# Performance work log

Measured on AMD Instinct MI355X. Metric: run time of the kernel, lower is better.

The kernel has to match this reference:

```python
import jax, jax.numpy as jnp
import numpy as np

BIG = 1e10
RADIUS = 0.5
NSAMPLE = 1


def square_distance(src, dst):
    # src: [B,N,3], dst: [B,M,3] -> [B,N,M] squared euclidean distances
    d = -2.0 * jnp.einsum('bnc,bmc->bnm', src, dst)
    d = d + jnp.sum(src ** 2, -1)[:, :, None]
    d = d + jnp.sum(dst ** 2, -1)[:, None, :]
    return d


def farthest_point_sample(xyz, npoint):
    # xyz: [B,N,3]; returns int32 indices [B,npoint]
    B, N, _ = xyz.shape
    dist0 = jnp.full((B, N), BIG, dtype=xyz.dtype)
    far0 = jnp.argmax(xyz[:, :, 0], axis=1).astype(jnp.int32)

    def step(carry, _):
        dist, far = carry
        centroid = jnp.take_along_axis(xyz, far[:, None, None], axis=1)  # [B,1,3]
        d = jnp.sum((xyz - centroid) ** 2, -1)  # [B,N]
        dist = jnp.minimum(dist, d)
        new_far = jnp.argmax(dist, axis=-1).astype(jnp.int32)
        return (dist, new_far), far  # record PRE-update farthest, like the torch loop

    (_, _), centroids = jax.lax.scan(step, (dist0, far0), None, length=npoint)
    return centroids.T  # [B,npoint]


def index_points(points, idx):
    # points: [B,N,C], idx: [B,S] -> [B,S,C]
    return jnp.take_along_axis(points, idx[:, :, None], axis=1)


def query_ball_point(radius, nsample, xyz, new_xyz):
    # xyz: [B,N,3], new_xyz: [B,S,3] -> int32 [B,S,nsample]
    B, S, _ = new_xyz.shape
    N = xyz.shape[1]
    sqrdists = square_distance(new_xyz, xyz)  # [B,S,N]
    base = jnp.arange(N, dtype=jnp.int32)
    group_idx = jnp.where(sqrdists > radius ** 2, jnp.int32(N), base)  # [B,S,N]
    group_idx = jnp.sort(group_idx, axis=-1)[:, :, :nsample]
    group_first = jnp.broadcast_to(group_idx[:, :, :1], group_idx.shape)
    group_idx = jnp.where(group_idx == N, group_first, group_idx)
    return group_idx


def setup_inputs() -> dict:
    key = jax.random.key(0)
    k1, k2 = jax.random.split(key)
    B, N = 4, 16384
    xyz = jax.random.uniform(k1, (B, 3, N), dtype=jnp.float32)
    cls_label = jax.random.uniform(k2, (B, 16), dtype=jnp.float32)
    return {"xyz": xyz, "cls_label": cls_label, "npoint": 1024}


def reference(xyz, cls_label, npoint):
    pts = jnp.transpose(xyz, (0, 2, 1))  # [B,N,3]
    centroids = farthest_point_sample(pts, npoint)  # [B,S]
    new_xyz = index_points(pts, centroids)  # [B,S,3]
    idx = query_ball_point(RADIUS, NSAMPLE, pts, new_xyz)  # [B,S,1]
    return idx
```

## Files before the change

kernel.cpp:

```cpp
#include <hip/hip_runtime.h>


constexpr int N_PTS  = 16384;
constexpr int NPOINT = 1024;
constexpr int BLOCK  = 512;
constexpr int KPT    = N_PTS / BLOCK;
constexpr int KP2    = KPT / 2;
constexpr int NWAVE  = BLOCK / 64;

typedef float f32x2 __attribute__((ext_vector_type(2)));

__device__ inline f32x2 pk_add(f32x2 a, f32x2 b) {
    f32x2 d;
    asm("v_pk_add_f32 %0, %1, %2" : "=v"(d) : "v"(a), "v"(b));
    return d;
}
__device__ inline f32x2 pk_mul(f32x2 a, f32x2 b) {
    f32x2 d;
    asm("v_pk_mul_f32 %0, %1, %2" : "=v"(d) : "v"(a), "v"(b));
    return d;
}

__device__ inline unsigned long long pack_key(float v, int idx) {
    return ((unsigned long long)__float_as_uint(v) << 32) |
           (unsigned)(N_PTS - 1 - idx);
}
__device__ inline int key_idx(unsigned long long k) {
    return N_PTS - 1 - (int)(k & 0xFFFFu);
}
__device__ inline unsigned long long umax64(unsigned long long a,
                                            unsigned long long b) {
    return a > b ? a : b;
}

__global__ __launch_bounds__(BLOCK, 2) void fps_kernel(
    const float* __restrict__ xyz,
    int* __restrict__ cent)
{
    const int b   = blockIdx.x;
    const int tid = threadIdx.x;
    const float* X = xyz + (size_t)b * 3 * N_PTS;
    const float* Y = X + N_PTS;
    const float* Z = X + 2 * N_PTS;

    f32x2 px[KP2], py[KP2], pz[KP2], dd[KP2];
#pragma unroll
    for (int k = 0; k < KP2; ++k) {
        const int p0 = tid + (2 * k) * BLOCK;
        const int p1 = tid + (2 * k + 1) * BLOCK;
        px[k] = f32x2{X[p0], X[p1]};
        py[k] = f32x2{Y[p0], Y[p1]};
        pz[k] = f32x2{Z[p0], Z[p1]};
        dd[k] = f32x2{1e10f, 1e10f};
    }
#pragma unroll
    for (int k = 0; k < KP2; ++k)
        asm("" : "+v"(px[k]), "+v"(py[k]), "+v"(pz[k]));

    __shared__ unsigned long long s_key[2][NWAVE];

    const int wave = tid >> 6;
    const int lane = tid & 63;

    int far;
    {
        float bv = px[0].x;
        int   bk = 0;
#pragma unroll
        for (int k = 0; k < KP2; ++k) {
            if (px[k].x > bv) { bv = px[k].x; bk = 2 * k; }
            if (px[k].y > bv) { bv = px[k].y; bk = 2 * k + 1; }
        }
        unsigned long long key = pack_key(bv, tid + bk * BLOCK);
#pragma unroll
        for (int off = 32; off > 0; off >>= 1)
            key = umax64(key, __shfl_xor(key, off));
        if (lane == 0) s_key[0][wave] = key;
        __syncthreads();
        const unsigned long long* sk = s_key[0];
        const unsigned long long bkk =
            umax64(umax64(umax64(sk[0], sk[1]), umax64(sk[2], sk[3])),
                   umax64(umax64(sk[4], sk[5]), umax64(sk[6], sk[7])));
        far = __builtin_amdgcn_readfirstlane(key_idx(bkk));
    }

    for (int it = 0; it < NPOINT; ++it) {
        if (tid == 0) cent[b * NPOINT + it] = far;
        if (it == NPOINT - 1) break;

        const float cx = X[far];
        const float cy = Y[far];
        const float cz = Z[far];
        const f32x2 ncx = {-cx, -cx};
        const f32x2 ncy = {-cy, -cy};
        const f32x2 ncz = {-cz, -cz};

        float nbv = -1.0f;
        int   nbk = 0;
#pragma unroll
        for (int k = 0; k < KP2; ++k) {
            const f32x2 dx = pk_add(px[k], ncx);
            const f32x2 dy = pk_add(py[k], ncy);
            const f32x2 dz = pk_add(pz[k], ncz);
            const f32x2 d  = pk_add(pk_add(pk_mul(dx, dx), pk_mul(dy, dy)),
                                    pk_mul(dz, dz));
            const float n0 = fminf(dd[k].x, d.x);
            const float n1 = fminf(dd[k].y, d.y);
            dd[k].x = n0;
            dd[k].y = n1;
            if (n0 > nbv) { nbv = n0; nbk = 2 * k; }
            if (n1 > nbv) { nbv = n1; nbk = 2 * k + 1; }
        }

        unsigned long long key = pack_key(nbv, tid + nbk * BLOCK);
#pragma unroll
        for (int off = 32; off > 0; off >>= 1)
            key = umax64(key, __shfl_xor(key, off));
        const int buf = (it + 1) & 1;
        if (lane == 0) s_key[buf][wave] = key;
        __syncthreads();

        const unsigned long long* sk = s_key[buf];
        const unsigned long long bkk =
            umax64(umax64(umax64(sk[0], sk[1]), umax64(sk[2], sk[3])),
                   umax64(umax64(sk[4], sk[5]), umax64(sk[6], sk[7])));
        far = __builtin_amdgcn_readfirstlane(key_idx(bkk));
    }
}

__global__ __launch_bounds__(256) void ballq_kernel(
    const float* __restrict__ xyz,
    const int* __restrict__ cent,
    int* __restrict__ out)
{
    const int gw   = (blockIdx.x * 256 + threadIdx.x) >> 6;
    const int lane = threadIdx.x & 63;
    const int b = gw / NPOINT;
    const int s = gw % NPOINT;

    const float* X = xyz + (size_t)b * 3 * N_PTS;
    const float* Y = X + N_PTS;
    const float* Z = X + 2 * N_PTS;

    const int ci = cent[b * NPOINT + s];
    const float cx = X[ci];
    const float cy = Y[ci];
    const float cz = Z[ci];
    const float cn = __fadd_rn(
        __fadd_rn(__fmul_rn(cx, cx), __fmul_rn(cy, cy)), __fmul_rn(cz, cz));

    int res = N_PTS;
    for (int base = 0; base < N_PTS; base += 64) {
        const int p = base + lane;
        const float x = X[p];
        const float y = Y[p];
        const float z = Z[p];
        const float dot = __fadd_rn(
            __fadd_rn(__fmul_rn(x, cx), __fmul_rn(y, cy)), __fmul_rn(z, cz));
        const float pn = __fadd_rn(
            __fadd_rn(__fmul_rn(x, x), __fmul_rn(y, y)), __fmul_rn(z, z));
        const float d = __fadd_rn(__fadd_rn(__fmul_rn(-2.0f, dot), cn), pn);
        const bool hit = !(d > 0.25f);
        const unsigned long long m = __ballot(hit);
        if (m) {
            res = base + (__ffsll((long long)m) - 1);
            break;
        }
    }
    if (lane == 0) out[b * NPOINT + s] = res;
}

extern "C" void kernel_launch(void* const* d_in, const int* in_sizes, int n_in,
                              void* d_out, int out_size, void* d_ws, size_t ws_size,
                              hipStream_t stream) {
    const float* xyz = (const float*)d_in[0];
    const int B = in_sizes[1] / 16;
    int* cent = (int*)d_ws;
    int* out  = (int*)d_out;

    fps_kernel<<<B, BLOCK, 0, stream>>>(xyz, cent);

    const int nwaves  = B * NPOINT;
    const int nblocks = nwaves / 4;
    ballq_kernel<<<nblocks, 256, 0, stream>>>(xyz, cent, out);
}
```

Baseline: 1.899 ms.

## Replace shuffle wave reduction with DPP max scan and split argmax chains

Replaces the six __shfl_xor 64-bit max-reduction steps in farthest point sampling with DPP row_shr/row_bcast steps, which avoid LDS-permute latency. The full wave result lands in lane 63. The per-thread argmax now uses two independent chains (even and odd slots) that are merged at the end, shortening the serial dependency in the inner loop. It also switches to the waves_per_eu attribute and masks indices defensively. DPP bank masks and lane ordering are subtle and could break tie-breaking if wrong.

```diff
diff --git a/kernel.cpp b/kernel.cpp
--- a/kernel.cpp
+++ b/kernel.cpp
@@ -33,7 +33,29 @@
     return a > b ? a : b;
 }
 
-__global__ __launch_bounds__(BLOCK, 2) void fps_kernel(
+template <int CTRL, int RM, int BM>
+__device__ inline unsigned long long dpp_max_step(unsigned long long key) {
+    const int lo = (int)(unsigned)key;
+    const int hi = (int)(unsigned)(key >> 32);
+    const unsigned mlo =
+        (unsigned)__builtin_amdgcn_update_dpp(lo, lo, CTRL, RM, BM, false);
+    const unsigned mhi =
+        (unsigned)__builtin_amdgcn_update_dpp(hi, hi, CTRL, RM, BM, false);
+    const unsigned long long moved = ((unsigned long long)mhi << 32) | mlo;
+    return key > moved ? key : moved;
+}
+__device__ inline unsigned long long wave_max_key(unsigned long long key) {
+    key = dpp_max_step<0x111, 0xf, 0xf>(key);
+    key = dpp_max_step<0x112, 0xf, 0xf>(key);
+    key = dpp_max_step<0x114, 0xf, 0xe>(key);
+    key = dpp_max_step<0x118, 0xf, 0xc>(key);
+    key = dpp_max_step<0x142, 0xa, 0xf>(key);
+    key = dpp_max_step<0x143, 0xc, 0xf>(key);
+    return key;
+}
+
+__global__ __launch_bounds__(BLOCK)
+__attribute__((amdgpu_waves_per_eu(2, 2))) void fps_kernel(
     const float* __restrict__ xyz,
     int* __restrict__ cent)
 {
@@ -55,7 +77,7 @@
     }
 #pragma unroll
     for (int k = 0; k < KP2; ++k)
-        asm("" : "+v"(px[k]), "+v"(py[k]), "+v"(pz[k]));
+        asm volatile("" : "+v"(px[k]), "+v"(py[k]), "+v"(pz[k]));
 
     __shared__ unsigned long long s_key[2][NWAVE];
 
@@ -71,17 +93,16 @@
             if (px[k].x > bv) { bv = px[k].x; bk = 2 * k; }
             if (px[k].y > bv) { bv = px[k].y; bk = 2 * k + 1; }
         }
-        unsigned long long key = pack_key(bv, tid + bk * BLOCK);
-#pragma unroll
-        for (int off = 32; off > 0; off >>= 1)
-            key = umax64(key, __shfl_xor(key, off));
-        if (lane == 0) s_key[0][wave] = key;
+        const unsigned long long key =
+            wave_max_key(pack_key(bv, tid + bk * BLOCK));
+        if (lane == 63) s_key[0][wave] = key;
         __syncthreads();
         const unsigned long long* sk = s_key[0];
         const unsigned long long bkk =
             umax64(umax64(umax64(sk[0], sk[1]), umax64(sk[2], sk[3])),
                    umax64(umax64(sk[4], sk[5]), umax64(sk[6], sk[7])));
-        far = __builtin_amdgcn_readfirstlane(key_idx(bkk));
+        far = __builtin_amdgcn_readfirstlane(key_idx(bkk)) &
+              (N_PTS - 1);
     }
 
     for (int it = 0; it < NPOINT; ++it) {
@@ -95,8 +116,8 @@
         const f32x2 ncy = {-cy, -cy};
         const f32x2 ncz = {-cz, -cz};
 
-        float nbv = -1.0f;
-        int   nbk = 0;
+        float bv0 = -1.0f, bv1 = -1.0f;
+        int   k0  = 0,     k1  = 1;
 #pragma unroll
         for (int k = 0; k < KP2; ++k) {
             const f32x2 dx = pk_add(px[k], ncx);
@@ -108,23 +129,26 @@
             const float n1 = fminf(dd[k].y, d.y);
             dd[k].x = n0;
             dd[k].y = n1;
-            if (n0 > nbv) { nbv = n0; nbk = 2 * k; }
-            if (n1 > nbv) { nbv = n1; nbk = 2 * k + 1; }
+            if (n0 > bv0) { bv0 = n0; k0 = 2 * k; }
+            if (n1 > bv1) { bv1 = n1; k1 = 2 * k + 1; }
         }
-
-        unsigned long long key = pack_key(nbv, tid + nbk * BLOCK);
-#pragma unroll
-        for (int off = 32; off > 0; off >>= 1)
-            key = umax64(key, __shfl_xor(key, off));
+        float nbv;
+        int   nbk;
+        if (bv1 > bv0 || (bv1 == bv0 && k1 < k0)) { nbv = bv1; nbk = k1; }
+        else                                      { nbv = bv0; nbk = k0; }
+
+        const unsigned long long key =
+            wave_max_key(pack_key(nbv, tid + (nbk << 9)));
         const int buf = (it + 1) & 1;
-        if (lane == 0) s_key[buf][wave] = key;
+        if (lane == 63) s_key[buf][wave] = key;
         __syncthreads();
 
         const unsigned long long* sk = s_key[buf];
         const unsigned long long bkk =
             umax64(umax64(umax64(sk[0], sk[1]), umax64(sk[2], sk[3])),
                    umax64(umax64(sk[4], sk[5]), umax64(sk[6], sk[7])));
-        far = __builtin_amdgcn_readfirstlane(key_idx(bkk));
+        far = __builtin_amdgcn_readfirstlane(key_idx(bkk)) &
+              (N_PTS - 1);
     }
 }
 
@@ -142,7 +166,7 @@
     const float* Y = X + N_PTS;
     const float* Z = X + 2 * N_PTS;
 
-    const int ci = cent[b * NPOINT + s];
+    const int ci = cent[b * NPOINT + s] & (N_PTS - 1);
     const float cx = X[ci];
     const float cy = Y[ci];
     const float cz = Z[ci];
```

Measured after the change: 1.785 ms. -6.0%, faster.
